# Kernel tuning notes

Hardware: AMD Instinct MI355X
Metric: run time of the kernel (lower is better)

Reference implementation:

```python
import jax, jax.numpy as jnp
import numpy as np


def _lstm_scan(x, W, U, b):
    """Unidirectional Keras-style LSTM over x: [B, T, F] -> [B, T, H].
    Gate order (i, f, c, o); sigmoid recurrent activation, tanh activation."""
    B = x.shape[0]
    H = U.shape[0]
    # Precompute input projections for all timesteps: [B, T, 4H]
    xp = jnp.einsum('btf,fg->btg', x, W) + b

    def step(carry, xt):
        h, c = carry
        z = xt + h @ U  # [B, 4H]
        i, f, g, o = jnp.split(z, 4, axis=-1)
        i = jax.nn.sigmoid(i)
        f = jax.nn.sigmoid(f)
        g = jnp.tanh(g)
        o = jax.nn.sigmoid(o)
        c = f * c + i * g
        h = o * jnp.tanh(c)
        return (h, c), h

    init = (jnp.zeros((B, H), x.dtype), jnp.zeros((B, H), x.dtype))
    _, hs = jax.lax.scan(step, init, xp.transpose(1, 0, 2))  # [T, B, H]
    return hs.transpose(1, 0, 2)


def _bidir(x, Wf, Uf, bf, Wb, Ub, bb):
    fwd = _lstm_scan(x, Wf, Uf, bf)
    bwd = jnp.flip(_lstm_scan(jnp.flip(x, axis=1), Wb, Ub, bb), axis=1)
    return jnp.concatenate([fwd, bwd], axis=-1)  # merge_mode='concat'


def setup_inputs() -> dict:
    key = jax.random.key(0)
    ks = jax.random.split(key, 16)
    B, T, F, H = 64, 1024, 64, 256
    s_in0 = 1.0 / np.sqrt(F)
    s_in1 = 1.0 / np.sqrt(2 * H)
    s_rec = 1.0 / np.sqrt(H)
    inp = {
        'x': jax.random.normal(ks[0], (B, T, F), jnp.float32),
        'W0f': jax.random.normal(ks[1], (F, 4 * H), jnp.float32) * s_in0,
        'U0f': jax.random.normal(ks[2], (H, 4 * H), jnp.float32) * s_rec,
        'b0f': jnp.zeros((4 * H,), jnp.float32),
        'W0b': jax.random.normal(ks[3], (F, 4 * H), jnp.float32) * s_in0,
        'U0b': jax.random.normal(ks[4], (H, 4 * H), jnp.float32) * s_rec,
        'b0b': jnp.zeros((4 * H,), jnp.float32),
        'W1f': jax.random.normal(ks[5], (2 * H, 4 * H), jnp.float32) * s_in1,
        'U1f': jax.random.normal(ks[6], (H, 4 * H), jnp.float32) * s_rec,
        'b1f': jnp.zeros((4 * H,), jnp.float32),
        'W1b': jax.random.normal(ks[7], (2 * H, 4 * H), jnp.float32) * s_in1,
        'U1b': jax.random.normal(ks[8], (H, 4 * H), jnp.float32) * s_rec,
        'b1b': jnp.zeros((4 * H,), jnp.float32),
        'Wd': jax.random.normal(ks[9], (2 * H, 1), jnp.float32) * s_in1,
        'bd': jnp.zeros((1,), jnp.float32),
    }
    return inp


def reference(x, W0f, U0f, b0f, W0b, U0b, b0b,
              W1f, U1f, b1f, W1b, U1b, b1b, Wd, bd):
    # Layer 0 bidirectional LSTM -> [B, T, 2H]; dropout is identity at inference
    h = _bidir(x, W0f, U0f, b0f, W0b, U0b, b0b)
    # Layer 1 bidirectional LSTM -> [B, T, 2H]
    h = _bidir(h, W1f, U1f, b1f, W1b, U1b, b1b)
    # Dense(1, linear) head -> [B, T, 1]
    return jnp.einsum('btd,do->bto', h, Wd) + bd
```

## Files before the change

### kernel.cpp

```cpp
#include <hip/hip_runtime.h>
#include <hip/hip_bf16.h>
#include <cstdint>
#include <cstddef>

#define B_ 64
#define T_ 1024

typedef _Float16 half_t;
typedef __attribute__((ext_vector_type(8))) _Float16 half8;
typedef __attribute__((ext_vector_type(4))) float f32x4;
typedef __attribute__((ext_vector_type(8))) unsigned short ushort8;

__device__ __forceinline__ float sigm(float x) { return 1.f / (1.f + __expf(-x)); }
__device__ __forceinline__ float tanh_fast(float x) {
  float e = __expf(2.f * x);
  return 1.f - 2.f / (e + 1.f);
}

__global__ __launch_bounds__(256) void permute_cols(const float* __restrict__ src,
                                                    float* __restrict__ dst, int K) {
  int idx = blockIdx.x * 256 + threadIdx.x;
  if (idx >= K * 1024) return;
  int n = idx & 1023;
  size_t k = (size_t)(idx >> 10);
  dst[idx] = src[(k << 10) + ((size_t)(n & 3) << 8) + (n >> 2)];
}

__global__ __launch_bounds__(256) void pack_u_mfma(const float* __restrict__ src,
                                                   half_t* __restrict__ dst) {
  int tid = blockIdx.x * 256 + threadIdx.x;
  int l = tid & 63;
  int s = (tid >> 6) & 7;
  int n = (tid >> 9) & 1;
  int w = (tid >> 10) & 3;
  int wgc = (tid >> 12) & 7;
  int col = wgc * 128 + w * 32 + n * 16 + (l & 15);
  int hc = col >> 2, g = col & 3;
  int k0 = s * 32 + (l >> 4) * 8;
  half8 v;
#pragma unroll
  for (int j = 0; j < 8; ++j)
    v[j] = (half_t)src[(size_t)(k0 + j) * 1024 + (g << 8) + hc];
  *(half8*)(dst + (size_t)tid * 8) = v;
}

__global__ __launch_bounds__(256) void pack_w0_mfma(const float* __restrict__ src,
                                                    half_t* __restrict__ dst) {
  int line = blockIdx.x * 256 + threadIdx.x;
  int l = line & 63;
  int ks = (line >> 6) & 1;
  int n = (line >> 7) & 1;
  int w = (line >> 8) & 3;
  int wgc = (line >> 10) & 7;
  int col = wgc * 128 + w * 32 + n * 16 + (l & 15);
  int sc = ((col & 3) << 8) + (col >> 2);
  int k0 = ks * 32 + (l >> 4) * 8;
  half8 v;
#pragma unroll
  for (int j = 0; j < 8; ++j)
    v[j] = (half_t)src[(size_t)(k0 + j) * 1024 + sc];
  *(half8*)(dst + (size_t)line * 8) = v;
}

__global__ __launch_bounds__(256) void pack_w1_mfma(const float* __restrict__ src,
                                                    half_t* __restrict__ dst) {
  int tid = blockIdx.x * 256 + threadIdx.x;
  int l = tid & 63;
  int ks = (tid >> 6) & 15;
  int nb = tid >> 10;
  int colp = nb * 16 + (l & 15);
  int sc = ((colp & 3) << 8) + (colp >> 2);
  int k0 = ks * 32 + (l >> 4) * 8;
  half8 v;
#pragma unroll
  for (int j = 0; j < 8; ++j)
    v[j] = (half_t)src[(size_t)(k0 + j) * 1024 + sc];
  *(half8*)(dst + (size_t)tid * 8) = v;
}

__global__ __launch_bounds__(256) void pack_x_f16(const float* __restrict__ x,
                                                  unsigned short* __restrict__ xi) {
  int idx = blockIdx.x * 256 + threadIdx.x;
  int b = idx & 15;
  int q = (idx >> 4) & 3;
  int ks = (idx >> 6) & 1;
  int t = (idx >> 7) & 1023;
  int bg = idx >> 17;
  const float* src = x + ((size_t)(bg * 16 + b) * T_ + t) * 64 + ks * 32 + q * 8;
  ushort8 v;
#pragma unroll
  for (int j = 0; j < 8; ++j) {
    half_t h = (half_t)src[j];
    v[j] = __builtin_bit_cast(unsigned short, h);
  }
  *(ushort8*)(xi + (size_t)idx * 8) = v;
}

__global__ __launch_bounds__(256) void init_out(float* __restrict__ out,
                                                const float* __restrict__ bd, int n) {
  int i = blockIdx.x * 256 + threadIdx.x;
  if (i < n) out[i] = bd[0];
}

__global__ __launch_bounds__(256) void diag_out(float* __restrict__ out, int n, float v) {
  int i = blockIdx.x * 256 + threadIdx.x;
  if (i < n) out[i] = (i == 0) ? v : 0.f;
}

__global__ __launch_bounds__(256) void proj1_mfma(
    const unsigned short* __restrict__ h0,
    const half_t* __restrict__ Wf, const half_t* __restrict__ Wb,
    const float* __restrict__ bpf, const float* __restrict__ bpb,
    float* __restrict__ xp, int s0, int Tc) {
  const int dir = blockIdx.z;
  const half_t* Wpk = dir ? Wb : Wf;
  const float* bs = dir ? bpb : bpf;
  const int b = blockIdx.y;
  const int mt = blockIdx.x;
  const int tid = threadIdx.x;
  const int l = tid & 63, w = tid >> 6;

  __shared__ __align__(16) unsigned short A_lds[16][520];

  {
    int r = tid >> 4, c16 = tid & 15;
    int sl = mt * 16 + r;
    int t = dir ? (T_ - 1 - s0 - sl) : (s0 + sl);
    const ushort8* srcp =
        (const ushort8*)(h0 + ((size_t)b * T_ + t) * 512 + c16 * 32);
#pragma unroll
    for (int u = 0; u < 4; ++u)
      *(ushort8*)&A_lds[r][c16 * 32 + u * 8] = __builtin_nontemporal_load(srcp + u);
  }
  __syncthreads();

  f32x4 acc[16];
#pragma unroll
  for (int n = 0; n < 16; ++n) acc[n] = (f32x4){0.f, 0.f, 0.f, 0.f};

  for (int ks = 0; ks < 16; ++ks) {
    half8 a = *(const half8*)&A_lds[l & 15][ks * 32 + (l >> 4) * 8];
    const half_t* bp_ = Wpk + (((size_t)(w * 16) * 16 + ks) * 64 + l) * 8;
#pragma unroll
    for (int n = 0; n < 16; ++n) {
      half8 bfr = *(const half8*)(bp_ + (size_t)n * 16 * 64 * 8);
      acc[n] = __builtin_amdgcn_mfma_f32_16x16x32_f16(a, bfr, acc[n], 0, 0, 0);
    }
  }

#pragma unroll
  for (int n = 0; n < 16; ++n) {
    int col = (w * 16 + n) * 16 + (l & 15);
    float bias = bs[col];
#pragma unroll
    for (int r = 0; r < 4; ++r) {
      int sl = mt * 16 + (l >> 4) * 4 + r;
      __builtin_nontemporal_store(
          acc[n][r] + bias,
          &xp[(((size_t)dir * B_ + b) * Tc + sl) * 1024 + col]);
    }
  }
}

template <int L0>
__global__ __launch_bounds__(512, 1) void lstm_scan_mfma(
    const float* __restrict__ xp,
    const unsigned short* __restrict__ xi,
    const half_t* __restrict__ W0f_, const half_t* __restrict__ W0b_,
    const float* __restrict__ b0f_, const float* __restrict__ b0b_,
    const half_t* __restrict__ Upk_f, const half_t* __restrict__ Upk_b,
    float* __restrict__ carry_c,
    unsigned* __restrict__ payl, unsigned* __restrict__ flagw,
    int s0, int Tc, int tagbase,
    unsigned short* __restrict__ hout,
    const float* __restrict__ Wd, float* __restrict__ out) {
  const int blk = blockIdx.x;
  const int unit = blk & 7;
  const int wgc = blk >> 3;
  const int dir = unit & 1;
  const int bg = unit >> 1;
  const int b0u = bg * 16;
  const int tid = threadIdx.x;
  const int l = tid & 63;
  const int w8 = tid >> 6;
  const int wgco = wgc * 2 + (w8 >> 2);
  const int w = w8 & 3;

  __shared__ __align__(16) unsigned short A_lds[4096];
  __shared__ __align__(16) unsigned short hstage[1024];
  __shared__ float red_sm[128];

  const half_t* Upk = dir ? Upk_b : Upk_f;
  half8 U[2][8];
  {
    const half_t* up = Upk + (size_t)(wgco * 4 + w) * 8192;
#pragma unroll
    for (int n = 0; n < 2; ++n)
#pragma unroll
      for (int s = 0; s < 8; ++s)
        U[n][s] = *(const half8*)(up + ((size_t)(n * 8 + s) * 64 + l) * 8);
  }

  const int b_lane = 4 * (l >> 4) + (l & 3);
  const int hcb = wgco * 32 + w * 8 + ((l >> 2) & 3);
  const int colb = wgco * 128 + w * 32 + (l & 15);
  float cst[2];
#pragma unroll
  for (int n = 0; n < 2; ++n)
    cst[n] = (s0 == 0) ? 0.f
        : carry_c[((size_t)dir * B_ + b0u + b_lane) * 256 + hcb + n * 4];

  float wdl[2] = {0.f, 0.f};
  half8 W0r[2][2];
  float bias0[2] = {0.f, 0.f};
  const unsigned short* xib = nullptr;
  if (L0) {
    const half_t* W0pk = dir ? W0b_ : W0f_;
    const float* bs0 = dir ? b0b_ : b0f_;
#pragma unroll
    for (int n = 0; n < 2; ++n) {
      bias0[n] = bs0[colb + n * 16];
#pragma unroll
      for (int ks = 0; ks < 2; ++ks)
        W0r[n][ks] = *(const half8*)(W0pk +
            ((size_t)(((wgco * 4 + w) * 2 + n) * 2 + ks) * 64 + l) * 8);
    }
    xib = xi + (size_t)bg * T_ * 1024;
  } else {
    wdl[0] = Wd[dir * 256 + hcb];
    wdl[1] = Wd[dir * 256 + hcb + 4];
  }

  unsigned* payl_u = payl + (size_t)unit * 4096;
  unsigned* flag_u = flagw + unit * 16;

  if (s0 == 0) {
#pragma unroll
    for (int i = 0; i < 4; ++i) ((unsigned*)A_lds)[tid * 4 + i] = 0u;
  } else {
    unsigned dd[4];
#pragma unroll
    for (int i = 0; i < 4; ++i)
      dd[i] = __hip_atomic_load(payl_u + 2048 + tid * 4 + i,
                                __ATOMIC_RELAXED, __HIP_MEMORY_SCOPE_AGENT);
#pragma unroll
    for (int i = 0; i < 4; ++i)
      ((unsigned*)A_lds)[tid * 4 + i] = dd[i];
  }
  __syncthreads();

  const float* xpu = L0 ? nullptr : (xp + (size_t)(dir * B_ + b0u) * Tc * 1024);

  float xpre[2][4];
  half8 xfre[2];
  {
    if (L0) {
      int t0f = dir ? (T_ - 1 - s0) : s0;
#pragma unroll
      for (int ks = 0; ks < 2; ++ks)
        xfre[ks] = __builtin_nontemporal_load(
            (const half8*)((const half_t*)xib + (size_t)t0f * 1024 +
                           ((ks * 4 + (l >> 4)) * 16 + (l & 15)) * 8));
    } else {
#pragma unroll
      for (int n = 0; n < 2; ++n)
#pragma unroll
        for (int r = 0; r < 4; ++r)
          xpre[n][r] = __builtin_nontemporal_load(
              &xpu[((size_t)(4 * (l >> 4) + r) * Tc) * 1024 + colb + n * 16]);
    }
  }

  const int hbl = (w8 >> 2) * 512 + (w * 16 + b_lane) * 8 + ((l >> 2) & 3);

  for (int sl = 0; sl < Tc; ++sl) {
    const int s = s0 + sl;
    const int t = dir ? (T_ - 1 - s) : s;
    const int slot = s & 1;

    f32x4 acc[2];
    if (L0) {
#pragma unroll
      for (int n = 0; n < 2; ++n)
#pragma unroll
        for (int r = 0; r < 4; ++r) acc[n][r] = bias0[n];
      half8 xa0 = xfre[0], xa1 = xfre[1];
#pragma unroll
      for (int n = 0; n < 2; ++n) {
        acc[n] = __builtin_amdgcn_mfma_f32_16x16x32_f16(xa0, W0r[n][0], acc[n], 0, 0, 0);
        acc[n] = __builtin_amdgcn_mfma_f32_16x16x32_f16(xa1, W0r[n][1], acc[n], 0, 0, 0);
      }
    } else {
#pragma unroll
      for (int n = 0; n < 2; ++n)
#pragma unroll
        for (int r = 0; r < 4; ++r) acc[n][r] = xpre[n][r];
    }

    half8 a[8];
#pragma unroll
    for (int sK = 0; sK < 8; ++sK)
      a[sK] = *(const half8*)&((const half_t*)A_lds)[((sK * 4 + (l >> 4)) * 16 + (l & 15)) * 8];

#pragma unroll
    for (int sK = 0; sK < 8; ++sK) {
      acc[0] = __builtin_amdgcn_mfma_f32_16x16x32_f16(a[sK], U[0][sK], acc[0], 0, 0, 0);
      acc[1] = __builtin_amdgcn_mfma_f32_16x16x32_f16(a[sK], U[1][sK], acc[1], 0, 0, 0);
    }

    float vhead = 0.f;
    unsigned short hu2[2];
#pragma unroll
    for (int n = 0; n < 2; ++n) {
      float v0 = acc[n][0], v1 = acc[n][1], v2 = acc[n][2], v3 = acc[n][3];
      float x0 = __shfl_xor(v1, 1), x1 = __shfl_xor(v0, 1);
      float x2 = __shfl_xor(v3, 1), x3 = __shfl_xor(v2, 1);
      float a0 = (l & 1) ? x0 : v0;
      float a1 = (l & 1) ? v1 : x1;
      float a2 = (l & 1) ? x2 : v2;
      float a3 = (l & 1) ? v3 : x3;
      float y0 = __shfl_xor(a2, 2), y1 = __shfl_xor(a3, 2);
      float y2 = __shfl_xor(a0, 2), y3 = __shfl_xor(a1, 2);
      float u0 = (l & 2) ? y0 : a0;
      float u1 = (l & 2) ? y1 : a1;
      float u2 = (l & 2) ? a2 : y2;
      float u3 = (l & 2) ? a3 : y3;

      float iG = sigm(u0), fG = sigm(u1), gG = tanh_fast(u2), oG = sigm(u3);
      float cn = fG * cst[n] + iG * gG;
      cst[n] = cn;
      float h = oG * tanh_fast(cn);

      if (!L0) vhead += h * wdl[n];
      hu2[n] = __builtin_bit_cast(unsigned short, (half_t)h);
      if (sl == Tc - 1)
        carry_c[((size_t)dir * B_ + b0u + b_lane) * 256 + hcb + n * 4] = cn;
    }
    hstage[hbl] = hu2[0];
    hstage[hbl + 4] = hu2[1];
    if (!L0) {
      vhead += __shfl_xor(vhead, 4);
      vhead += __shfl_xor(vhead, 8);
      if ((l & 12) == 0) red_sm[w8 * 16 + b_lane] = vhead;
    }
    __syncthreads();

    const unsigned* hs32 = (const unsigned*)hstage;
    __hip_atomic_store(payl_u + slot * 2048 + wgc * 512 + tid, hs32[tid],
                       __ATOMIC_RELAXED, __HIP_MEMORY_SCOPE_AGENT);

    asm volatile("s_waitcnt vmcnt(0)" ::: "memory");
    __syncthreads();
    const unsigned want = (unsigned)(tagbase + s + 1);
    if (tid == 0)
      __hip_atomic_store(flag_u + slot * 8 + wgc, want,
                         __ATOMIC_RELAXED, __HIP_MEMORY_SCOPE_AGENT);

    if (L0) {
      int sub = tid >> 8, r = tid & 255;
      int bb = r >> 4, cc = r & 15;
      __builtin_nontemporal_store(
          hs32[sub * 256 + (cc >> 2) * 64 + bb * 4 + (cc & 3)],
          (unsigned*)hout + ((size_t)(b0u + bb) * T_ + t) * 256 + dir * 128 +
              (wgc * 2 + sub) * 16 + cc);
    } else if (tid < 16) {
      float sum = ((red_sm[tid] + red_sm[16 + tid]) +
                   (red_sm[32 + tid] + red_sm[48 + tid])) +
                  ((red_sm[64 + tid] + red_sm[80 + tid]) +
                   (red_sm[96 + tid] + red_sm[112 + tid]));
      atomicAdd(out + (((size_t)(b0u + tid)) << 10) + t, sum);
    }

    if (sl + 1 < Tc) {
      if (L0) {
        int tn = dir ? (T_ - 2 - s) : (s + 1);
#pragma unroll
        for (int ks = 0; ks < 2; ++ks)
          xfre[ks] = __builtin_nontemporal_load(
              (const half8*)((const half_t*)xib + (size_t)tn * 1024 +
                             ((ks * 4 + (l >> 4)) * 16 + (l & 15)) * 8));
      } else {
#pragma unroll
        for (int n = 0; n < 2; ++n)
#pragma unroll
          for (int r = 0; r < 4; ++r)
            xpre[n][r] = __builtin_nontemporal_load(
                &xpu[((size_t)(4 * (l >> 4) + r) * Tc + sl + 1) * 1024 + colb + n * 16]);
      }

      if (tid < 4 && tid != wgc) {
        while (__hip_atomic_load(flag_u + slot * 8 + tid, __ATOMIC_RELAXED,
                                 __HIP_MEMORY_SCOPE_AGENT) != want) {}
      }
      __syncthreads();
      unsigned dd[4];
      const int g = tid >> 6;
      if ((g >> 1) == wgc) {
#pragma unroll
        for (int i = 0; i < 4; ++i)
          dd[i] = hs32[(g & 1) * 256 + (tid & 63) * 4 + i];
      } else {
#pragma unroll
        for (int i = 0; i < 4; ++i)
          dd[i] = __hip_atomic_load(payl_u + slot * 2048 + tid * 4 + i,
                                    __ATOMIC_RELAXED, __HIP_MEMORY_SCOPE_AGENT);
      }
#pragma unroll
      for (int i = 0; i < 4; ++i)
        ((unsigned*)A_lds)[tid * 4 + i] = dd[i];
      __syncthreads();
    }
  }
}

extern "C" void kernel_launch(void* const* d_in, const int* in_sizes, int n_in,
                              void* d_out, int out_size, void* d_ws, size_t ws_size,
                              hipStream_t stream) {
  const float* x   = (const float*)d_in[0];
  const float* W0f = (const float*)d_in[1];
  const float* U0f = (const float*)d_in[2];
  const float* b0f = (const float*)d_in[3];
  const float* W0b = (const float*)d_in[4];
  const float* U0b = (const float*)d_in[5];
  const float* b0b = (const float*)d_in[6];
  const float* W1f = (const float*)d_in[7];
  const float* U1f = (const float*)d_in[8];
  const float* b1f = (const float*)d_in[9];
  const float* W1b = (const float*)d_in[10];
  const float* U1b = (const float*)d_in[11];
  const float* b1b = (const float*)d_in[12];
  const float* Wd  = (const float*)d_in[13];
  const float* bd  = (const float*)d_in[14];
  float* out = (float*)d_out;
  char* ws = (char*)d_ws;

  const size_t H0_BYTES   = (size_t)B_ * T_ * 512 * 2;
  const size_t UPK_BYTES  = (size_t)262144 * 2;
  const size_t W0PK_BYTES = (size_t)8192 * 8 * 2;
  const size_t W1PK_BYTES = (size_t)512 * 1024 * 2;
  const size_t XI_BYTES   = (size_t)B_ * T_ * 64 * 2;
  const size_t BP_BYTES   = 1024 * 4;
  const size_t CC_BYTES   = (size_t)2 * B_ * 256 * 4;
  const size_t PL_BYTES   = (size_t)8 * 4096 * 4;
  const size_t FL_BYTES   = 1024;
  const size_t REPACK = 4 * UPK_BYTES + 2 * W0PK_BYTES + 2 * W1PK_BYTES +
                        XI_BYTES + 4 * BP_BYTES + CC_BYTES + PL_BYTES +
                        FL_BYTES + 1024;

  int Tc = 0;
  for (int tc = 256; tc >= 64; tc >>= 1) {
    size_t xpb = (size_t)2 * B_ * tc * 1024 * 4;
    if (H0_BYTES + REPACK + xpb <= ws_size) { Tc = tc; break; }
  }
  if (!Tc) {
    float v = 1000.f + (float)(ws_size >> 20);
    diag_out<<<(out_size + 255) / 256, 256, 0, stream>>>(out, out_size, v);
    return;
  }

  size_t off = 0;
  unsigned short* h0 = (unsigned short*)(ws + off); off += H0_BYTES;
  half_t* Up00 = (half_t*)(ws + off); off += UPK_BYTES;
  half_t* Up01 = (half_t*)(ws + off); off += UPK_BYTES;
  half_t* Up10 = (half_t*)(ws + off); off += UPK_BYTES;
  half_t* Up11 = (half_t*)(ws + off); off += UPK_BYTES;
  half_t* W0pf = (half_t*)(ws + off); off += W0PK_BYTES;
  half_t* W0pb = (half_t*)(ws + off); off += W0PK_BYTES;
  half_t* W1pf = (half_t*)(ws + off); off += W1PK_BYTES;
  half_t* W1pb = (half_t*)(ws + off); off += W1PK_BYTES;
  unsigned short* xi = (unsigned short*)(ws + off); off += XI_BYTES;
  float* bp0f = (float*)(ws + off); off += BP_BYTES;
  float* bp0b = (float*)(ws + off); off += BP_BYTES;
  float* bp1f = (float*)(ws + off); off += BP_BYTES;
  float* bp1b = (float*)(ws + off); off += BP_BYTES;
  float* carry_c = (float*)(ws + off); off += CC_BYTES;
  unsigned* payl = (unsigned*)(ws + off); off += PL_BYTES;
  unsigned* flagw = (unsigned*)(ws + off); off += FL_BYTES;
  off = (off + 255) & ~(size_t)255;
  float* xpc = (float*)(ws + off);

  pack_u_mfma<<<128, 256, 0, stream>>>(U0f, Up00);
  pack_u_mfma<<<128, 256, 0, stream>>>(U0b, Up01);
  pack_u_mfma<<<128, 256, 0, stream>>>(U1f, Up10);
  pack_u_mfma<<<128, 256, 0, stream>>>(U1b, Up11);
  pack_w0_mfma<<<32, 256, 0, stream>>>(W0f, W0pf);
  pack_w0_mfma<<<32, 256, 0, stream>>>(W0b, W0pb);
  pack_w1_mfma<<<256, 256, 0, stream>>>(W1f, W1pf);
  pack_w1_mfma<<<256, 256, 0, stream>>>(W1b, W1pb);
  pack_x_f16<<<2048, 256, 0, stream>>>(x, xi);
  permute_cols<<<4, 256, 0, stream>>>(b0f, bp0f, 1);
  permute_cols<<<4, 256, 0, stream>>>(b0b, bp0b, 1);
  permute_cols<<<4, 256, 0, stream>>>(b1f, bp1f, 1);
  permute_cols<<<4, 256, 0, stream>>>(b1b, bp1b, 1);

  lstm_scan_mfma<1><<<32, 512, 0, stream>>>(
      nullptr, xi, W0pf, W0pb, bp0f, bp0b, Up00, Up01, carry_c,
      payl, flagw, 0, T_, 0, h0, nullptr, nullptr);

  init_out<<<(out_size + 255) / 256, 256, 0, stream>>>(out, bd, out_size);
  const int nch = T_ / Tc;
  const dim3 pgrid(Tc / 16, B_, 2);
  for (int ci = 0; ci < nch; ++ci) {
    int s0c = ci * Tc;
    proj1_mfma<<<pgrid, 256, 0, stream>>>(h0, W1pf, W1pb, bp1f, bp1b,
                                          xpc, s0c, Tc);
    lstm_scan_mfma<0><<<32, 512, 0, stream>>>(
        xpc, nullptr, nullptr, nullptr, nullptr, nullptr, Up10, Up11, carry_c,
        payl, flagw, s0c, Tc, 1024, nullptr, Wd, out);
  }
}
```

Measured before the change: 6.438 ms.

## Overlap layer-1 input projection of next chunk with current scan

Adds extra blocks to the layer-1 scan launch that compute the input projection for the next time chunk into a double buffer, so the projection GEMM runs on idle CUs while the 32-block latency-bound recurrent scan proceeds. The chunk size is capped at 128 to fit two projection buffers. This removes the serial proj1 launch per chunk but relies on the scan blocks (which spin on flags) being scheduled alongside the projection blocks, and adds more chunks and launches.

```diff
diff --git a/kernel.cpp b/kernel.cpp
--- a/kernel.cpp
+++ b/kernel.cpp
@@ -173,22 +173,79 @@
     unsigned* __restrict__ payl, unsigned* __restrict__ flagw,
     int s0, int Tc, int tagbase,
     unsigned short* __restrict__ hout,
-    const float* __restrict__ Wd, float* __restrict__ out) {
+    const float* __restrict__ Wd, float* __restrict__ out,
+    const unsigned short* __restrict__ h0src,
+    const half_t* __restrict__ W1f_, const half_t* __restrict__ W1b_,
+    const float* __restrict__ bp1f_, const float* __restrict__ bp1b_,
+    float* __restrict__ xpn, int s0p) {
+  __shared__ __align__(16) unsigned short shmem[16 * 520];
+  const int tid = threadIdx.x;
+
+  if (!L0 && blockIdx.x >= 32) {
+    unsigned short(*A2)[520] = (unsigned short(*)[520])shmem;
+    int pb = blockIdx.x - 32;
+    int mpt = Tc / 16;
+    int mt = pb % mpt;
+    int b = (pb / mpt) % B_;
+    int dir = pb / (mpt * B_);
+    const half_t* Wpk = dir ? W1b_ : W1f_;
+    const float* bs = dir ? bp1b_ : bp1f_;
+    const int l = tid & 63, w = tid >> 6;
+
+    if (tid < 256) {
+      int r = tid >> 4, c16 = tid & 15;
+      int sl = mt * 16 + r;
+      int t = dir ? (T_ - 1 - s0p - sl) : (s0p + sl);
+      const ushort8* srcp =
+          (const ushort8*)(h0src + ((size_t)b * T_ + t) * 512 + c16 * 32);
+#pragma unroll
+      for (int u = 0; u < 4; ++u)
+        *(ushort8*)&A2[r][c16 * 32 + u * 8] = __builtin_nontemporal_load(srcp + u);
+    }
+    __syncthreads();
+    if (tid < 256) {
+      f32x4 acc[16];
+#pragma unroll
+      for (int n = 0; n < 16; ++n) acc[n] = (f32x4){0.f, 0.f, 0.f, 0.f};
+      for (int ks = 0; ks < 16; ++ks) {
+        half8 a = *(const half8*)&A2[l & 15][ks * 32 + (l >> 4) * 8];
+        const half_t* bp_ = Wpk + (((size_t)(w * 16) * 16 + ks) * 64 + l) * 8;
+#pragma unroll
+        for (int n = 0; n < 16; ++n) {
+          half8 bfr = *(const half8*)(bp_ + (size_t)n * 16 * 64 * 8);
+          acc[n] = __builtin_amdgcn_mfma_f32_16x16x32_f16(a, bfr, acc[n], 0, 0, 0);
+        }
+      }
+#pragma unroll
+      for (int n = 0; n < 16; ++n) {
+        int col = (w * 16 + n) * 16 + (l & 15);
+        float bias = bs[col];
+#pragma unroll
+        for (int r = 0; r < 4; ++r) {
+          int sl = mt * 16 + (l >> 4) * 4 + r;
+          __builtin_nontemporal_store(
+              acc[n][r] + bias,
+              &xpn[(((size_t)dir * B_ + b) * Tc + sl) * 1024 + col]);
+        }
+      }
+    }
+    return;
+  }
+
+  unsigned short* A_lds = shmem;
+  unsigned short* hstage = shmem + 4096;
+  float* red_sm = (float*)(shmem + 5120);
+
   const int blk = blockIdx.x;
   const int unit = blk & 7;
   const int wgc = blk >> 3;
   const int dir = unit & 1;
   const int bg = unit >> 1;
   const int b0u = bg * 16;
-  const int tid = threadIdx.x;
   const int l = tid & 63;
   const int w8 = tid >> 6;
   const int wgco = wgc * 2 + (w8 >> 2);
   const int w = w8 & 3;
-
-  __shared__ __align__(16) unsigned short A_lds[4096];
-  __shared__ __align__(16) unsigned short hstage[1024];
-  __shared__ float red_sm[128];
 
   const half_t* Upk = dir ? Upk_b : Upk_f;
   half8 U[2][8];
@@ -448,15 +505,16 @@
                         FL_BYTES + 1024;
 
   int Tc = 0;
-  for (int tc = 256; tc >= 64; tc >>= 1) {
+  for (int tc = 128; tc >= 64; tc >>= 1) {
     size_t xpb = (size_t)2 * B_ * tc * 1024 * 4;
-    if (H0_BYTES + REPACK + xpb <= ws_size) { Tc = tc; break; }
+    if (H0_BYTES + REPACK + 2 * xpb <= ws_size) { Tc = tc; break; }
   }
   if (!Tc) {
     float v = 1000.f + (float)(ws_size >> 20);
     diag_out<<<(out_size + 255) / 256, 256, 0, stream>>>(out, out_size, v);
     return;
   }
+  const size_t XP_BYTES = (size_t)2 * B_ * Tc * 1024 * 4;
 
   size_t off = 0;
   unsigned short* h0 = (unsigned short*)(ws + off); off += H0_BYTES;
@@ -477,7 +535,8 @@
   unsigned* payl = (unsigned*)(ws + off); off += PL_BYTES;
   unsigned* flagw = (unsigned*)(ws + off); off += FL_BYTES;
   off = (off + 255) & ~(size_t)255;
-  float* xpc = (float*)(ws + off);
+  float* xpA = (float*)(ws + off); off += XP_BYTES;
+  float* xpB = (float*)(ws + off);
 
   pack_u_mfma<<<128, 256, 0, stream>>>(U0f, Up00);
   pack_u_mfma<<<128, 256, 0, stream>>>(U0b, Up01);
@@ -495,17 +554,22 @@
 
   lstm_scan_mfma<1><<<32, 512, 0, stream>>>(
       nullptr, xi, W0pf, W0pb, bp0f, bp0b, Up00, Up01, carry_c,
-      payl, flagw, 0, T_, 0, h0, nullptr, nullptr);
+      payl, flagw, 0, T_, 0, h0, nullptr, nullptr,
+      nullptr, nullptr, nullptr, nullptr, nullptr, nullptr, 0);
 
   init_out<<<(out_size + 255) / 256, 256, 0, stream>>>(out, bd, out_size);
   const int nch = T_ / Tc;
-  const dim3 pgrid(Tc / 16, B_, 2);
+  const int nproj = (Tc / 16) * B_ * 2;
+  proj1_mfma<<<dim3(Tc / 16, B_, 2), 256, 0, stream>>>(
+      h0, W1pf, W1pb, bp1f, bp1b, xpA, 0, Tc);
   for (int ci = 0; ci < nch; ++ci) {
     int s0c = ci * Tc;
-    proj1_mfma<<<pgrid, 256, 0, stream>>>(h0, W1pf, W1pb, bp1f, bp1b,
-                                          xpc, s0c, Tc);
-    lstm_scan_mfma<0><<<32, 512, 0, stream>>>(
-        xpc, nullptr, nullptr, nullptr, nullptr, nullptr, Up10, Up11, carry_c,
-        payl, flagw, s0c, Tc, 1024, nullptr, Wd, out);
-  }
-}
+    float* xcur = (ci & 1) ? xpB : xpA;
+    float* xnext = (ci & 1) ? xpA : xpB;
+    int extra = (ci + 1 < nch) ? nproj : 0;
+    lstm_scan_mfma<0><<<32 + extra, 512, 0, stream>>>(
+        xcur, nullptr, nullptr, nullptr, nullptr, nullptr, Up10, Up11, carry_c,
+        payl, flagw, s0c, Tc, 1024, nullptr, Wd, out,
+        h0, W1pf, W1pb, bp1f, bp1b, xnext, (ci + 1) * Tc);
+  }
+}
```

Measured after the change: 5.928 ms (median of 2 runs). 7.9% less time.
